# Kernel optimization log

Hardware: AMD Instinct MI355X
Metric: run time of the kernel (lower is better)

Reference implementation:

```python
import jax, jax.numpy as jnp
import numpy as np

B, S, T, D, H_HEADS = 2, 2048, 2048, 1024, 16
HD = D // H_HEADS
EPS = 1e-5


def _ln(x, g, b):
    m = jnp.mean(x, axis=-1, keepdims=True)
    v = jnp.mean(jnp.square(x - m), axis=-1, keepdims=True)
    return g * (x - m) * jax.lax.rsqrt(v + EPS) + b


def _mha(xq, xkv, Wq, bq, Wk, bk, Wv, bv, Wo, bo, causal):
    Bq, Lq, _ = xq.shape
    Lk = xkv.shape[1]
    q = (xq @ Wq + bq).reshape(Bq, Lq, H_HEADS, HD)
    k = (xkv @ Wk + bk).reshape(Bq, Lk, H_HEADS, HD)
    v = (xkv @ Wv + bv).reshape(Bq, Lk, H_HEADS, HD)
    scores = jnp.einsum('bqhd,bkhd->bhqk', q, k) / jnp.sqrt(jnp.asarray(HD, q.dtype))
    if causal:
        mask = jnp.tril(jnp.ones((Lq, Lk), dtype=bool))
        scores = jnp.where(mask, scores, jnp.asarray(-1e9, scores.dtype))
    p = jax.nn.softmax(scores, axis=-1)
    o = jnp.einsum('bhqk,bkhd->bqhd', p, v).reshape(Bq, Lq, D)
    return o @ Wo + bo


def setup_inputs() -> dict:
    key = jax.random.key(0)
    ks = jax.random.split(key, 24)
    s = 0.02
    def w(i):
        return jax.random.normal(ks[i], (D, D), jnp.float32) * s
    inp = {
        'S0': jax.random.normal(ks[20], (B, S, D), jnp.float32),
        'H': jax.random.normal(ks[21], (B, T, D), jnp.float32),
        'Wq1': w(0), 'bq1': jnp.zeros((D,)), 'Wk1': w(1), 'bk1': jnp.zeros((D,)),
        'Wv1': w(2), 'bv1': jnp.zeros((D,)), 'Wo1': w(3), 'bo1': jnp.zeros((D,)),
        'ln1_g': jnp.ones((D,)), 'ln1_b': jnp.zeros((D,)),
        'Wq2': w(4), 'bq2': jnp.zeros((D,)), 'Wk2': w(5), 'bk2': jnp.zeros((D,)),
        'Wv2': w(6), 'bv2': jnp.zeros((D,)), 'Wo2': w(7), 'bo2': jnp.zeros((D,)),
        'ln2_g': jnp.ones((D,)), 'ln2_b': jnp.zeros((D,)),
        'Wf': w(8), 'bf': jnp.zeros((D,)),
        'ln3_g': jnp.ones((D,)), 'ln3_b': jnp.zeros((D,)),
    }
    return inp


def reference(S0, H, Wq1, bq1, Wk1, bk1, Wv1, bv1, Wo1, bo1, ln1_g, ln1_b,
              Wq2, bq2, Wk2, bk2, Wv2, bv2, Wo2, bo2, ln2_g, ln2_b,
              Wf, bf, ln3_g, ln3_b):
    # masked (causal) self-attention + add&norm
    a1 = _mha(S0, S0, Wq1, bq1, Wk1, bk1, Wv1, bv1, Wo1, bo1, causal=True)
    S1 = _ln(S0 + a1, ln1_g, ln1_b)
    # cross-attention over encoder output H + add&norm
    a2 = _mha(S1, H, Wq2, bq2, Wk2, bk2, Wv2, bv2, Wo2, bo2, causal=False)
    S2 = _ln(S1 + a2, ln2_g, ln2_b)
    # FFN (single Linear) + add&norm
    S3 = _ln(S2 + (S2 @ Wf + bf), ln3_g, ln3_b)
    return S3
```

## Files before the change

kernel.cpp:

```cpp
#include <hip/hip_runtime.h>
#include <hip/hip_bf16.h>
#include <cstdint>
#include <cstddef>


#define D_DIM 1024
#define SEQ   2048
#define NHEAD 16
#define HDIM  64
#define MROWS 4096

typedef __attribute__((ext_vector_type(8)))  short bf16x8;
typedef __attribute__((ext_vector_type(4)))  float f32x4;
typedef __attribute__((ext_vector_type(16))) float f32x16;
typedef __attribute__((ext_vector_type(4)))  unsigned int u32x4;

static __device__ __forceinline__ short f2bf(float x) {
    __hip_bfloat16 h = __float2bfloat16(x);
    return *reinterpret_cast<short*>(&h);
}

static __device__ __forceinline__ unsigned int cvtpk(float lo, float hi2) {
    unsigned int r;
    asm("v_cvt_pk_bf16_f32 %0, %1, %2" : "=v"(r) : "v"(lo), "v"(hi2));
    return r;
}

#define GLOAD_LDS16(g, l)                                                     \
    __builtin_amdgcn_global_load_lds(                                         \
        (const __attribute__((address_space(1))) unsigned int*)(g),           \
        (__attribute__((address_space(3))) unsigned int*)(l), 16, 0, 0)

struct WPtrs { const float* p[9]; };

__global__ __launch_bounds__(256) void prep_kernel(
    WPtrs wp, short* __restrict__ Wt,
    const float* __restrict__ s0, const float* __restrict__ hx,
    short* __restrict__ d0, short* __restrict__ d1,
    const float* __restrict__ bq1, const float* __restrict__ bk1,
    const float* __restrict__ bv1, const float* __restrict__ bk2,
    const float* __restrict__ bv2, float* __restrict__ cb1,
    float* __restrict__ cb2)
{
    __shared__ float tl[64][65];
    const int t = threadIdx.x;
    const int id = blockIdx.x;
    if (id < 2304) {
        const int z = id >> 8, rem = id & 255;
        const float* src = wp.p[z];
        short* dst = Wt + (size_t)z * D_DIM * D_DIM;
        const int r0 = (rem >> 4) * 64;
        const int c0 = (rem & 15) * 64;
        #pragma unroll
        for (int i = 0; i < 4; ++i) {
            int row = i * 16 + (t >> 4);
            int col = (t & 15) * 4;
            float4 v = *(const float4*)(src + (size_t)(r0 + row) * D_DIM + c0 + col);
            tl[row][col + 0] = v.x; tl[row][col + 1] = v.y;
            tl[row][col + 2] = v.z; tl[row][col + 3] = v.w;
        }
        __syncthreads();
        #pragma unroll
        for (int i = 0; i < 4; ++i) {
            int nrow = i * 16 + (t >> 4);
            int kcol = (t & 15) * 4;
            ushort4 o;
            o.x = (unsigned short)f2bf(tl[kcol + 0][nrow]);
            o.y = (unsigned short)f2bf(tl[kcol + 1][nrow]);
            o.z = (unsigned short)f2bf(tl[kcol + 2][nrow]);
            o.w = (unsigned short)f2bf(tl[kcol + 3][nrow]);
            *(ushort4*)(dst + (size_t)(c0 + nrow) * D_DIM + r0 + kcol) = o;
        }
    } else if (id < 6400) {
        const int cid = id - 2304;
        const bool second = cid >= 2048;
        const float* src = second ? hx : s0;
        short* dst = second ? d1 : d0;
        size_t i = ((size_t)(cid - (second ? 2048 : 0)) * 256 + t) * 8;
        float4 a = *(const float4*)(src + i);
        float4 b = *(const float4*)(src + i + 4);
        bf16x8 o;
        o[0] = f2bf(a.x); o[1] = f2bf(a.y); o[2] = f2bf(a.z); o[3] = f2bf(a.w);
        o[4] = f2bf(b.x); o[5] = f2bf(b.y); o[6] = f2bf(b.z); o[7] = f2bf(b.w);
        *(bf16x8*)(dst + i) = o;
    } else {
        const int i = (id - 6400) * 256 + t;
        if      (i < 1024) cb1[i] = bq1[i];
        else if (i < 2048) cb1[i] = bk1[i - 1024];
        else if (i < 3072) cb1[i] = bv1[i - 2048];
        else if (i < 4096) cb2[i - 3072] = bk2[i - 3072];
        else               cb2[i - 3072] = bv2[i - 4096];
    }
}

__device__ __forceinline__ void gemm_qkv_body(
    short* __restrict__ As_, short* __restrict__ Bs_,
    const short* __restrict__ A, const short* __restrict__ Bt,
    const float* __restrict__ bias,
    short* __restrict__ Qh, short* __restrict__ Kh, short* __restrict__ Vh,
    int col0, float qscale, int bx, int by)
{
    const int t = threadIdx.x;
    const int wave = t >> 6, lane = t & 63;
    const int wm = wave >> 1, wn = wave & 1;
    const int m0 = bx * 128, n0 = by * 128;
    const int l15 = lane & 15, l4 = lane >> 4;
    const int lrow = lane >> 2, lcol = (lane & 3) * 8;
    f32x4 acc[4][4] = {};
    for (int k0 = 0; k0 < D_DIM; k0 += 32) {
        __syncthreads();
        #pragma unroll
        for (int c = 0; c < 2; ++c) {
            int chunk = wave + c * 4;
            int row = chunk * 16 + lrow;
            GLOAD_LDS16(A  + (size_t)(m0 + row) * D_DIM + k0 + lcol,
                        As_ + chunk * 512 + lane * 8);
            GLOAD_LDS16(Bt + (size_t)(n0 + row) * D_DIM + k0 + lcol,
                        Bs_ + chunk * 512 + lane * 8);
        }
        __syncthreads();
        bf16x8 af[4], bfr[4];
        const int kq = l4 * 8;
        #pragma unroll
        for (int i = 0; i < 4; ++i)
            af[i] = *(const bf16x8*)&As_[(wm * 64 + i * 16 + l15) * 32 + kq];
        #pragma unroll
        for (int j = 0; j < 4; ++j)
            bfr[j] = *(const bf16x8*)&Bs_[(wn * 64 + j * 16 + l15) * 32 + kq];
        #pragma unroll
        for (int i = 0; i < 4; ++i)
            #pragma unroll
            for (int j = 0; j < 4; ++j)
                acc[i][j] = __builtin_amdgcn_mfma_f32_16x16x32_bf16(
                    af[i], bfr[j], acc[i][j], 0, 0, 0);
    }
    const int rbase = m0 + wm * 64;
    const int cbase = n0 + wn * 64;
    float bv[4];
    #pragma unroll
    for (int j = 0; j < 4; ++j) bv[j] = bias[cbase + j * 16 + l15];
    #pragma unroll
    for (int i = 0; i < 4; ++i) {
        #pragma unroll
        for (int r = 0; r < 4; ++r) {
            const int grow = rbase + i * 16 + l4 * 4 + r;
            const int b = grow >> 11, s = grow & 2047;
            #pragma unroll
            for (int j = 0; j < 4; ++j) {
                const int vcol = col0 + cbase + j * 16 + l15;
                float v = acc[i][j][r] + bv[j];
                if (vcol < 1024) v *= qscale;
                short* dst = (vcol < 1024) ? Qh : ((vcol < 2048) ? Kh : Vh);
                const int h = (vcol >> 6) & 15, hd = vcol & 63;
                dst[((size_t)(b * 16 + h) * SEQ + s) * HDIM + hd] = f2bf(v);
            }
        }
    }
}

__global__ __launch_bounds__(256) void gemm_qkv_kernel(
    const short* __restrict__ A, const short* __restrict__ Bt,
    const float* __restrict__ bias,
    short* __restrict__ Qh, short* __restrict__ Kh, short* __restrict__ Vh,
    int col0, float qscale)
{
    __shared__ short lds[8192];
    gemm_qkv_body(lds, lds + 4096, A, Bt, bias, Qh, Kh, Vh,
                  col0, qscale, blockIdx.x, blockIdx.y);
}

__global__ __launch_bounds__(256) void gemm_resid_kernel(
    const short* __restrict__ A, const short* __restrict__ Bt,
    const float* __restrict__ bias, const float* __restrict__ resid,
    float* __restrict__ Cout)
{
    __shared__ short As[128 * 32];
    __shared__ short Bs[64 * 32];
    const int t = threadIdx.x;
    const int wave = t >> 6, lane = t & 63;
    const int wm = wave >> 1, wn = wave & 1;
    const int m0 = blockIdx.x * 128, n0 = blockIdx.y * 64;
    const int l15 = lane & 15, l4 = lane >> 4;
    const int lrow = lane >> 2, lcol = (lane & 3) * 8;
    f32x4 acc[4][2] = {};
    for (int k0 = 0; k0 < D_DIM; k0 += 32) {
        __syncthreads();
        #pragma unroll
        for (int c = 0; c < 2; ++c) {
            int chunk = wave + c * 4;
            int row = chunk * 16 + lrow;
            GLOAD_LDS16(A + (size_t)(m0 + row) * D_DIM + k0 + lcol,
                        As + chunk * 512 + lane * 8);
        }
        {
            int row = wave * 16 + lrow;
            GLOAD_LDS16(Bt + (size_t)(n0 + row) * D_DIM + k0 + lcol,
                        Bs + wave * 512 + lane * 8);
        }
        __syncthreads();
        bf16x8 af[4], bfr[2];
        const int kq = l4 * 8;
        #pragma unroll
        for (int i = 0; i < 4; ++i)
            af[i] = *(const bf16x8*)&As[(wm * 64 + i * 16 + l15) * 32 + kq];
        #pragma unroll
        for (int j = 0; j < 2; ++j)
            bfr[j] = *(const bf16x8*)&Bs[(wn * 32 + j * 16 + l15) * 32 + kq];
        #pragma unroll
        for (int i = 0; i < 4; ++i)
            #pragma unroll
            for (int j = 0; j < 2; ++j)
                acc[i][j] = __builtin_amdgcn_mfma_f32_16x16x32_bf16(
                    af[i], bfr[j], acc[i][j], 0, 0, 0);
    }
    const int rbase = m0 + wm * 64;
    const int cbase = n0 + wn * 32;
    float bv[2];
    #pragma unroll
    for (int j = 0; j < 2; ++j) bv[j] = bias[cbase + j * 16 + l15];
    #pragma unroll
    for (int i = 0; i < 4; ++i) {
        #pragma unroll
        for (int r = 0; r < 4; ++r) {
            const int grow = rbase + i * 16 + l4 * 4 + r;
            #pragma unroll
            for (int j = 0; j < 2; ++j) {
                const int gcol = cbase + j * 16 + l15;
                float v = acc[i][j][r] + bv[j]
                        + resid[(size_t)grow * D_DIM + gcol];
                Cout[(size_t)grow * D_DIM + gcol] = v;
            }
        }
    }
}

template<bool CAUSAL>
__device__ __forceinline__ void attn_body(
    char* ldsb,
    const short* __restrict__ Qh, const short* __restrict__ Kh,
    const short* __restrict__ Vh, short* __restrict__ O, const int id)
{
    const int t = threadIdx.x, wave = t >> 6, lane = t & 63;
    const int q_own = lane & 31, hi = lane >> 5;
    const int bh = ((id & 7) << 2) | ((id >> 3) & 3);
    const int qsel = id >> 5;
    const int b = bh >> 4, h = bh & 15;
    const short* Qp = Qh + (size_t)bh * SEQ * HDIM;
    const short* Kp = Kh + (size_t)bh * SEQ * HDIM;
    const short* Vp = Vh + (size_t)bh * SEQ * HDIM;
    short* Op = O + (size_t)b * SEQ * D_DIM + h * HDIM;

    const int ksrc = (t & 7) ^ ((t >> 3) & 7);
    const int vr2 = (t & 31) * 2, vg = (t >> 5) * 8;
    const int swz = (q_own & 7) << 3;

    bf16x8 ones;
    #pragma unroll
    for (int j = 0; j < 8; ++j) ones[j] = (short)0x3F80;

    const int npm = CAUSAL ? 2 : 1;
    for (int pm = 0; pm < npm; ++pm) {
        const int qt = CAUSAL ? (pm == 0 ? qsel : 15 - qsel) : qsel;
        const int q0 = qt * 128;
        const int qw = q0 + wave * 32;

        bf16x8 qf[4];
        #pragma unroll
        for (int s = 0; s < 4; ++s)
            qf[s] = *(const bf16x8*)(Qp + (size_t)(qw + q_own) * HDIM
                                     + s * 16 + hi * 8);

        int qkb[4], pvb[8], vwb[8], kgb;
        #pragma unroll
        for (int s = 0; s < 4; ++s)
            qkb[s] = q_own * 128 + 2 * ((s * 16 + hi * 8) ^ swz);
        #pragma unroll
        for (int ks = 0; ks < 8; ++ks)
            pvb[ks] = 32768 + q_own * 256 + 2 * ((ks * 16 + hi * 8) ^ swz);
        #pragma unroll
        for (int j = 0; j < 8; ++j)
            vwb[j] = 32768 + (vg + j) * 256 + 2 * (vr2 ^ (j << 3));
        kgb = t * 16;

        f32x16 oacc[2] = {};
        f32x16 lsum = {};
        float m_ = 0.0f;
        const int nkt = CAUSAL ? (qt + 1) : (SEQ / 128);
        u32x4 pawp[8];

        bf16x8 va0, vb0, va1, vb1;

        if (pm) __syncthreads();

        #pragma unroll
        for (int c = 0; c < 4; ++c) {
            const int row = c * 32 + (t >> 3);
            GLOAD_LDS16(Kp + (size_t)row * HDIM + ksrc * 8,
                        ldsb + kgb + c * 4096);
        }
        va0 = *(const bf16x8*)(Vp + (size_t)vr2 * HDIM + vg);
        vb0 = *(const bf16x8*)(Vp + (size_t)(vr2 + 1) * HDIM + vg);
        va1 = *(const bf16x8*)(Vp + (size_t)(64 + vr2) * HDIM + vg);
        vb1 = *(const bf16x8*)(Vp + (size_t)(65 + vr2) * HDIM + vg);
        #pragma unroll
        for (int j = 0; j < 8; ++j) {
            unsigned int p0 = ((unsigned int)(unsigned short)vb0[j] << 16)
                            | (unsigned short)va0[j];
            unsigned int p1 = ((unsigned int)(unsigned short)vb1[j] << 16)
                            | (unsigned short)va1[j];
            *(unsigned int*)(ldsb + vwb[j])       = p0;
            *(unsigned int*)(ldsb + vwb[j] + 128) = p1;
        }
        __syncthreads();
        kgb ^= 16384;
        #pragma unroll
        for (int j = 0; j < 8; ++j) vwb[j] ^= 16384;

        for (int kt = 0; kt < nkt; ++kt) {
            const int kbase = kt * 128;
            const bool have_next = (kt + 1 < nkt);

            if (have_next) {
                #pragma unroll
                for (int c = 0; c < 4; ++c) {
                    const int row = kbase + 128 + c * 32 + (t >> 3);
                    GLOAD_LDS16(Kp + (size_t)row * HDIM + ksrc * 8,
                                ldsb + kgb + c * 4096);
                }
                va0 = *(const bf16x8*)(Vp + (size_t)(kbase + 128 + vr2) * HDIM + vg);
                vb0 = *(const bf16x8*)(Vp + (size_t)(kbase + 129 + vr2) * HDIM + vg);
                va1 = *(const bf16x8*)(Vp + (size_t)(kbase + 192 + vr2) * HDIM + vg);
                vb1 = *(const bf16x8*)(Vp + (size_t)(kbase + 193 + vr2) * HDIM + vg);
            }

            f32x16 minit;
            #pragma unroll
            for (int rr = 0; rr < 16; ++rr) minit[rr] = -m_;
            f32x16 sc[4];
            sc[0] = minit; sc[1] = minit; sc[2] = minit; sc[3] = minit;
            __builtin_amdgcn_s_setprio(1);
            #pragma unroll
            for (int kt2 = 0; kt2 < 4; ++kt2) {
                #pragma unroll
                for (int s = 0; s < 4; ++s) {
                    bf16x8 kf = *(const bf16x8*)(ldsb + qkb[s] + kt2 * 4096);
                    sc[kt2] = __builtin_amdgcn_mfma_f32_32x32x16_bf16(
                        kf, qf[s], sc[kt2], 0, 0, 0);
                }
            }

            if (kt > 0) {
                #pragma unroll
                for (int ks = 0; ks < 8; ++ks) {
                    union { u32x4 u; bf16x8 bv8; } pc;
                    pc.u = pawp[ks];
                    bf16x8 vf0 = *(const bf16x8*)(ldsb + (pvb[ks] ^ 16384));
                    oacc[0] = __builtin_amdgcn_mfma_f32_32x32x16_bf16(
                        vf0, pc.bv8, oacc[0], 0, 0, 0);
                    bf16x8 vf1 = *(const bf16x8*)(ldsb + (pvb[ks] ^ 16384) + 8192);
                    oacc[1] = __builtin_amdgcn_mfma_f32_32x32x16_bf16(
                        vf1, pc.bv8, oacc[1], 0, 0, 0);
                    lsum = __builtin_amdgcn_mfma_f32_32x32x16_bf16(
                        ones, pc.bv8, lsum, 0, 0, 0);
                }
            }
            __builtin_amdgcn_s_setprio(0);

            if (CAUSAL && (kbase + 127 > qw)) {
                #pragma unroll
                for (int kt2 = 0; kt2 < 4; ++kt2)
                    #pragma unroll
                    for (int rr = 0; rr < 16; ++rr) {
                        const int k = kbase + kt2 * 32
                                    + (rr & 3) + 8 * (rr >> 2) + 4 * hi;
                        if (k > qw + q_own) sc[kt2][rr] = -1e30f;
                    }
            }

            float km[4];
            #pragma unroll
            for (int kt2 = 0; kt2 < 4; ++kt2) {
                float t0 = fmaxf(fmaxf(sc[kt2][0],  sc[kt2][1]),  sc[kt2][2]);
                float t1 = fmaxf(fmaxf(sc[kt2][3],  sc[kt2][4]),  sc[kt2][5]);
                float t2 = fmaxf(fmaxf(sc[kt2][6],  sc[kt2][7]),  sc[kt2][8]);
                float t3 = fmaxf(fmaxf(sc[kt2][9],  sc[kt2][10]), sc[kt2][11]);
                float t4 = fmaxf(fmaxf(sc[kt2][12], sc[kt2][13]), sc[kt2][14]);
                float u  = fmaxf(fmaxf(t0, t1), t2);
                float v  = fmaxf(fmaxf(t3, t4), sc[kt2][15]);
                km[kt2] = fmaxf(u, v);
            }
            float smax = fmaxf(fmaxf(fmaxf(km[0], km[1]), km[2]), km[3]);
            smax = fmaxf(smax, __shfl_xor(smax, 32));

            if (!__all(smax <= 8.0f)) {
                const float sp = fmaxf(smax, 0.f);
                const float corr = exp2f(-sp);
                lsum[0] *= corr;
                #pragma unroll
                for (int ht = 0; ht < 2; ++ht)
                    #pragma unroll
                    for (int rr = 0; rr < 16; ++rr)
                        oacc[ht][rr] *= corr;
                #pragma unroll
                for (int kt2 = 0; kt2 < 4; ++kt2)
                    #pragma unroll
                    for (int rr = 0; rr < 16; ++rr)
                        sc[kt2][rr] -= sp;
                m_ += sp;
            }

            #pragma unroll
            for (int kt2 = 0; kt2 < 4; ++kt2)
                #pragma unroll
                for (int rr = 0; rr < 16; ++rr)
                    sc[kt2][rr] = exp2f(sc[kt2][rr]);

            #pragma unroll
            for (int kt2 = 0; kt2 < 4; ++kt2) {
                unsigned int w0a = cvtpk(sc[kt2][0],  sc[kt2][1]);
                unsigned int w0b = cvtpk(sc[kt2][2],  sc[kt2][3]);
                unsigned int w1a = cvtpk(sc[kt2][4],  sc[kt2][5]);
                unsigned int w1b = cvtpk(sc[kt2][6],  sc[kt2][7]);
                unsigned int w2a = cvtpk(sc[kt2][8],  sc[kt2][9]);
                unsigned int w2b = cvtpk(sc[kt2][10], sc[kt2][11]);
                unsigned int w3a = cvtpk(sc[kt2][12], sc[kt2][13]);
                unsigned int w3b = cvtpk(sc[kt2][14], sc[kt2][15]);
                asm("v_permlane32_swap_b32 %0, %1" : "+v"(w0a), "+v"(w1a));
                asm("v_permlane32_swap_b32 %0, %1" : "+v"(w0b), "+v"(w1b));
                asm("v_permlane32_swap_b32 %0, %1" : "+v"(w2a), "+v"(w3a));
                asm("v_permlane32_swap_b32 %0, %1" : "+v"(w2b), "+v"(w3b));
                pawp[kt2 * 2 + 0][0] = w0a; pawp[kt2 * 2 + 0][1] = w0b;
                pawp[kt2 * 2 + 0][2] = w1a; pawp[kt2 * 2 + 0][3] = w1b;
                pawp[kt2 * 2 + 1][0] = w2a; pawp[kt2 * 2 + 1][1] = w2b;
                pawp[kt2 * 2 + 1][2] = w3a; pawp[kt2 * 2 + 1][3] = w3b;
            }

            if (have_next) {
                __syncthreads();
                #pragma unroll
                for (int j = 0; j < 8; ++j) {
                    unsigned int p0 = ((unsigned int)(unsigned short)vb0[j] << 16)
                                    | (unsigned short)va0[j];
                    unsigned int p1 = ((unsigned int)(unsigned short)vb1[j] << 16)
                                    | (unsigned short)va1[j];
                    *(unsigned int*)(ldsb + vwb[j])       = p0;
                    *(unsigned int*)(ldsb + vwb[j] + 128) = p1;
                }
            }
            kgb ^= 16384;
            #pragma unroll
            for (int s = 0; s < 4; ++s) qkb[s] ^= 16384;
            #pragma unroll
            for (int ks = 0; ks < 8; ++ks) pvb[ks] ^= 16384;
            #pragma unroll
            for (int j = 0; j < 8; ++j) vwb[j] ^= 16384;
        }

        __builtin_amdgcn_s_setprio(1);
        #pragma unroll
        for (int ks = 0; ks < 8; ++ks) {
            union { u32x4 u; bf16x8 bv8; } pc;
            pc.u = pawp[ks];
            bf16x8 vf0 = *(const bf16x8*)(ldsb + (pvb[ks] ^ 16384));
            oacc[0] = __builtin_amdgcn_mfma_f32_32x32x16_bf16(
                vf0, pc.bv8, oacc[0], 0, 0, 0);
            bf16x8 vf1 = *(const bf16x8*)(ldsb + (pvb[ks] ^ 16384) + 8192);
            oacc[1] = __builtin_amdgcn_mfma_f32_32x32x16_bf16(
                vf1, pc.bv8, oacc[1], 0, 0, 0);
            lsum = __builtin_amdgcn_mfma_f32_32x32x16_bf16(
                ones, pc.bv8, lsum, 0, 0, 0);
        }
        __builtin_amdgcn_s_setprio(0);

        const float inv = 1.0f / lsum[0];
        const int grow = qw + q_own;
        #pragma unroll
        for (int ht = 0; ht < 2; ++ht)
            #pragma unroll
            for (int j = 0; j < 4; ++j) {
                ushort4 o;
                o.x = (unsigned short)f2bf(oacc[ht][4 * j + 0] * inv);
                o.y = (unsigned short)f2bf(oacc[ht][4 * j + 1] * inv);
                o.z = (unsigned short)f2bf(oacc[ht][4 * j + 2] * inv);
                o.w = (unsigned short)f2bf(oacc[ht][4 * j + 3] * inv);
                *(ushort4*)&Op[(size_t)grow * D_DIM + ht * 32 + 8 * j + 4 * hi] = o;
            }
    }
}

template<bool CAUSAL>
__global__ __launch_bounds__(256, 2) void attn_mfma_kernel(
    const short* __restrict__ Qh, const short* __restrict__ Kh,
    const short* __restrict__ Vh, short* __restrict__ O)
{
    __shared__ short lds[32768];
    attn_body<CAUSAL>((char*)lds, Qh, Kh, Vh, O, blockIdx.x);
}

__global__ __launch_bounds__(256, 2) void fused_cattn_kv2_kernel(
    const short* __restrict__ Qh, const short* __restrict__ Kh,
    const short* __restrict__ Vh, short* __restrict__ O,
    const short* __restrict__ A2, const short* __restrict__ Bt2,
    const float* __restrict__ bias2,
    short* __restrict__ Kh2, short* __restrict__ Vh2)
{
    __shared__ short lds[32768];
    if (blockIdx.x < 256) {
        attn_body<true>((char*)lds, Qh, Kh, Vh, O, blockIdx.x);
    } else {
        const int bx2 = blockIdx.x - 256;
        gemm_qkv_body(lds, lds + 4096, A2, Bt2, bias2,
                      nullptr, Kh2, Vh2, 1024, 1.0f, bx2 & 31, bx2 >> 5);
    }
}

__global__ __launch_bounds__(256) void ln_kernel(
    const float* __restrict__ X, const float* __restrict__ g,
    const float* __restrict__ bb, float* __restrict__ outf,
    short* __restrict__ outb)
{
    const int row = blockIdx.x;
    const int t = threadIdx.x;
    const float* x = X + (size_t)row * D_DIM;
    float4 v = *(const float4*)(x + (t << 2));
    float s  = v.x + v.y + v.z + v.w;
    float sq = v.x * v.x + v.y * v.y + v.z * v.z + v.w * v.w;
    #pragma unroll
    for (int off = 1; off < 64; off <<= 1) {
        s  += __shfl_xor(s, off);
        sq += __shfl_xor(sq, off);
    }
    __shared__ float ss[4], ssq[4];
    const int wid = t >> 6, lane = t & 63;
    if (lane == 0) { ss[wid] = s; ssq[wid] = sq; }
    __syncthreads();
    s  = ss[0] + ss[1] + ss[2] + ss[3];
    sq = ssq[0] + ssq[1] + ssq[2] + ssq[3];
    const float mean = s * (1.0f / 1024.0f);
    const float var  = sq * (1.0f / 1024.0f) - mean * mean;
    const float inv  = rsqrtf(var + 1e-5f);
    float4 gv = *(const float4*)(g  + (t << 2));
    float4 bv = *(const float4*)(bb + (t << 2));
    float4 o;
    o.x = gv.x * (v.x - mean) * inv + bv.x;
    o.y = gv.y * (v.y - mean) * inv + bv.y;
    o.z = gv.z * (v.z - mean) * inv + bv.z;
    o.w = gv.w * (v.w - mean) * inv + bv.w;
    if (outf) *(float4*)(outf + (size_t)row * D_DIM + (t << 2)) = o;
    if (outb) {
        ushort4 ob;
        ob.x = (unsigned short)f2bf(o.x); ob.y = (unsigned short)f2bf(o.y);
        ob.z = (unsigned short)f2bf(o.z); ob.w = (unsigned short)f2bf(o.w);
        *(ushort4*)(outb + (size_t)row * D_DIM + (t << 2)) = ob;
    }
}

extern "C" void kernel_launch(void* const* d_in, const int* in_sizes, int n_in,
                              void* d_out, int out_size, void* d_ws, size_t ws_size,
                              hipStream_t stream)
{
    (void)in_sizes; (void)n_in; (void)out_size; (void)ws_size;
    const float* S0f = (const float*)d_in[0];
    const float* Hf  = (const float*)d_in[1];
    const float* bq1 = (const float*)d_in[3];
    const float* bk1 = (const float*)d_in[5];
    const float* bv1 = (const float*)d_in[7];
    const float* bo1 = (const float*)d_in[9];
    const float* g1  = (const float*)d_in[10]; const float* b1 = (const float*)d_in[11];
    const float* bq2 = (const float*)d_in[13];
    const float* bk2 = (const float*)d_in[15];
    const float* bv2 = (const float*)d_in[17];
    const float* bo2 = (const float*)d_in[19];
    const float* g2  = (const float*)d_in[20]; const float* b2 = (const float*)d_in[21];
    const float* bff = (const float*)d_in[23];
    const float* g3  = (const float*)d_in[24]; const float* b3 = (const float*)d_in[25];

    char* ws = (char*)d_ws;
    size_t off = 0;
    auto alloc = [&](size_t bytes) { char* p = ws + off; off += (bytes + 255) & ~(size_t)255; return p; };
    short* Wt   = (short*)alloc((size_t)9 * D_DIM * D_DIM * 2);
    short* bS0  = (short*)alloc((size_t)MROWS * D_DIM * 2);
    short* bH   = (short*)alloc((size_t)MROWS * D_DIM * 2);
    short* Qhb  = (short*)alloc((size_t)MROWS * D_DIM * 2);
    short* Khb  = (short*)alloc((size_t)MROWS * D_DIM * 2);
    short* Vhb  = (short*)alloc((size_t)MROWS * D_DIM * 2);
    short* Khb2 = (short*)alloc((size_t)MROWS * D_DIM * 2);
    short* Vhb2 = (short*)alloc((size_t)MROWS * D_DIM * 2);
    short* bAO  = (short*)alloc((size_t)MROWS * D_DIM * 2);
    float* X    = (float*)alloc((size_t)MROWS * D_DIM * 4);
    short* bSx  = (short*)alloc((size_t)MROWS * D_DIM * 2);
    float* cb1  = (float*)alloc(3072 * 4);
    float* cb2  = (float*)alloc(2048 * 4);

    const size_t WSTRIDE = (size_t)D_DIM * D_DIM;
    const float QSCALE = 0.125f * 1.44269504088896f;

    WPtrs wp;
    wp.p[0] = (const float*)d_in[2];
    wp.p[1] = (const float*)d_in[4];
    wp.p[2] = (const float*)d_in[6];
    wp.p[3] = (const float*)d_in[8];
    wp.p[4] = (const float*)d_in[12];
    wp.p[5] = (const float*)d_in[14];
    wp.p[6] = (const float*)d_in[16];
    wp.p[7] = (const float*)d_in[18];
    wp.p[8] = (const float*)d_in[22];

    prep_kernel<<<dim3(6420), 256, 0, stream>>>(
        wp, Wt, S0f, Hf, bS0, bH, bq1, bk1, bv1, bk2, bv2, cb1, cb2);

    const dim3 blk(256);
    const dim3 attn_grid_f(512);
    const dim3 resid_grid(32, 16);

    gemm_qkv_kernel<<<dim3(32, 24), blk, 0, stream>>>(
        bS0, Wt, cb1, Qhb, Khb, Vhb, 0, QSCALE);
    fused_cattn_kv2_kernel<<<dim3(768), blk, 0, stream>>>(
        Qhb, Khb, Vhb, bAO, bH, Wt + 5 * WSTRIDE, cb2, Khb2, Vhb2);
    gemm_resid_kernel<<<resid_grid, blk, 0, stream>>>(
        bAO, Wt + 3 * WSTRIDE, bo1, S0f, X);
    ln_kernel<<<MROWS, blk, 0, stream>>>(X, g1, b1, X, bSx);

    gemm_qkv_kernel<<<dim3(32, 8), blk, 0, stream>>>(
        bSx, Wt + 4 * WSTRIDE, bq2, Qhb, Khb, Vhb, 0, QSCALE);
    attn_mfma_kernel<false><<<attn_grid_f, blk, 0, stream>>>(
        Qhb, Khb2, Vhb2, bAO);
    gemm_resid_kernel<<<resid_grid, blk, 0, stream>>>(
        bAO, Wt + 7 * WSTRIDE, bo2, X, X);
    ln_kernel<<<MROWS, blk, 0, stream>>>(X, g2, b2, X, bSx);

    gemm_resid_kernel<<<resid_grid, blk, 0, stream>>>(
        bSx, Wt + 8 * WSTRIDE, bff, X, X);
    ln_kernel<<<MROWS, blk, 0, stream>>>(X, g3, b3, (float*)d_out, nullptr);
}
```

Measured before the change: 288.0 us.

## Compute PV in the same iteration instead of deferring it one tile

Removes the software-pipelined schedule in the attention loop, where the P·V MFMAs for the previous key tile were issued right after the QK MFMAs of the current tile, followed by a tail PV after the loop. P·V is now computed straight after the softmax exponentials of the same tile, reading the current V buffer. The barrier moves from before the V staging writes to after them. This frees the pawp registers kept live across iterations and drops the epilogue, but the QK and PV matrix work no longer interleave with the softmax math.

```diff
diff --git a/kernel.cpp b/kernel.cpp
--- a/kernel.cpp
+++ b/kernel.cpp
@@ -286,7 +286,6 @@
         f32x16 lsum = {};
         float m_ = 0.0f;
         const int nkt = CAUSAL ? (qt + 1) : (SEQ / 128);
-        u32x4 pawp[8];
 
         bf16x8 va0, vb0, va1, vb1;
 
@@ -346,22 +345,6 @@
                     bf16x8 kf = *(const bf16x8*)(ldsb + qkb[s] + kt2 * 4096);
                     sc[kt2] = __builtin_amdgcn_mfma_f32_32x32x16_bf16(
                         kf, qf[s], sc[kt2], 0, 0, 0);
-                }
-            }
-
-            if (kt > 0) {
-                #pragma unroll
-                for (int ks = 0; ks < 8; ++ks) {
-                    union { u32x4 u; bf16x8 bv8; } pc;
-                    pc.u = pawp[ks];
-                    bf16x8 vf0 = *(const bf16x8*)(ldsb + (pvb[ks] ^ 16384));
-                    oacc[0] = __builtin_amdgcn_mfma_f32_32x32x16_bf16(
-                        vf0, pc.bv8, oacc[0], 0, 0, 0);
-                    bf16x8 vf1 = *(const bf16x8*)(ldsb + (pvb[ks] ^ 16384) + 8192);
-                    oacc[1] = __builtin_amdgcn_mfma_f32_32x32x16_bf16(
-                        vf1, pc.bv8, oacc[1], 0, 0, 0);
-                    lsum = __builtin_amdgcn_mfma_f32_32x32x16_bf16(
-                        ones, pc.bv8, lsum, 0, 0, 0);
                 }
             }
             __builtin_amdgcn_s_setprio(0);
@@ -415,6 +398,7 @@
                 for (int rr = 0; rr < 16; ++rr)
                     sc[kt2][rr] = exp2f(sc[kt2][rr]);
 
+            u32x4 paw[8];
             #pragma unroll
             for (int kt2 = 0; kt2 < 4; ++kt2) {
                 unsigned int w0a = cvtpk(sc[kt2][0],  sc[kt2][1]);
@@ -429,14 +413,29 @@
                 asm("v_permlane32_swap_b32 %0, %1" : "+v"(w0b), "+v"(w1b));
                 asm("v_permlane32_swap_b32 %0, %1" : "+v"(w2a), "+v"(w3a));
                 asm("v_permlane32_swap_b32 %0, %1" : "+v"(w2b), "+v"(w3b));
-                pawp[kt2 * 2 + 0][0] = w0a; pawp[kt2 * 2 + 0][1] = w0b;
-                pawp[kt2 * 2 + 0][2] = w1a; pawp[kt2 * 2 + 0][3] = w1b;
-                pawp[kt2 * 2 + 1][0] = w2a; pawp[kt2 * 2 + 1][1] = w2b;
-                pawp[kt2 * 2 + 1][2] = w3a; pawp[kt2 * 2 + 1][3] = w3b;
-            }
+                paw[kt2 * 2 + 0][0] = w0a; paw[kt2 * 2 + 0][1] = w0b;
+                paw[kt2 * 2 + 0][2] = w1a; paw[kt2 * 2 + 0][3] = w1b;
+                paw[kt2 * 2 + 1][0] = w2a; paw[kt2 * 2 + 1][1] = w2b;
+                paw[kt2 * 2 + 1][2] = w3a; paw[kt2 * 2 + 1][3] = w3b;
+            }
+
+            __builtin_amdgcn_s_setprio(1);
+            #pragma unroll
+            for (int ks = 0; ks < 8; ++ks) {
+                union { u32x4 u; bf16x8 bv8; } pc;
+                pc.u = paw[ks];
+                bf16x8 vf0 = *(const bf16x8*)(ldsb + pvb[ks]);
+                oacc[0] = __builtin_amdgcn_mfma_f32_32x32x16_bf16(
+                    vf0, pc.bv8, oacc[0], 0, 0, 0);
+                bf16x8 vf1 = *(const bf16x8*)(ldsb + pvb[ks] + 8192);
+                oacc[1] = __builtin_amdgcn_mfma_f32_32x32x16_bf16(
+                    vf1, pc.bv8, oacc[1], 0, 0, 0);
+                lsum = __builtin_amdgcn_mfma_f32_32x32x16_bf16(
+                    ones, pc.bv8, lsum, 0, 0, 0);
+            }
+            __builtin_amdgcn_s_setprio(0);
 
             if (have_next) {
-                __syncthreads();
                 #pragma unroll
                 for (int j = 0; j < 8; ++j) {
                     unsigned int p0 = ((unsigned int)(unsigned short)vb0[j] << 16)
@@ -446,6 +445,7 @@
                     *(unsigned int*)(ldsb + vwb[j])       = p0;
                     *(unsigned int*)(ldsb + vwb[j] + 128) = p1;
                 }
+                __syncthreads();
             }
             kgb ^= 16384;
             #pragma unroll
@@ -455,22 +455,6 @@
             #pragma unroll
             for (int j = 0; j < 8; ++j) vwb[j] ^= 16384;
         }
-
-        __builtin_amdgcn_s_setprio(1);
-        #pragma unroll
-        for (int ks = 0; ks < 8; ++ks) {
-            union { u32x4 u; bf16x8 bv8; } pc;
-            pc.u = pawp[ks];
-            bf16x8 vf0 = *(const bf16x8*)(ldsb + (pvb[ks] ^ 16384));
-            oacc[0] = __builtin_amdgcn_mfma_f32_32x32x16_bf16(
-                vf0, pc.bv8, oacc[0], 0, 0, 0);
-            bf16x8 vf1 = *(const bf16x8*)(ldsb + (pvb[ks] ^ 16384) + 8192);
-            oacc[1] = __builtin_amdgcn_mfma_f32_32x32x16_bf16(
-                vf1, pc.bv8, oacc[1], 0, 0, 0);
-            lsum = __builtin_amdgcn_mfma_f32_32x32x16_bf16(
-                ones, pc.bv8, lsum, 0, 0, 0);
-        }
-        __builtin_amdgcn_s_setprio(0);
 
         const float inv = 1.0f / lsum[0];
         const int grow = qw + q_own;
```

Result: faster. 275.6 us (median of 2 runs) (-4.3%).
